# Kernel tuning notes

Measured on AMD Instinct MI355X. Metric: run time of the kernel, lower is better.

The kernel has to match this reference:

```python
import jax, jax.numpy as jnp
import numpy as np

B, C, H, W, P = 16, 512, 64, 64, 32


def setup_inputs() -> dict:
    key = jax.random.key(0)
    k1, k2, k3 = jax.random.split(key, 3)
    inputs = jax.random.normal(k1, (B, C, H, W), dtype=jnp.float32)
    weight = jax.random.uniform(k2, (P, C, 1, 1), dtype=jnp.float32)
    smooth_factor = jax.random.normal(k3, (P,), dtype=jnp.float32)
    return {"inputs": inputs, "weight": weight, "smooth_factor": smooth_factor}


def reference(inputs, weight, smooth_factor):
    b, c, h, w = inputs.shape
    p = weight.shape[0]
    n = h * w
    centers = weight.reshape(p, c)                      # [P,C]
    x = inputs.reshape(b, c, n)                         # [B,C,N]

    # distance-based logits: 2<c,x> - |x|^2 - |c|^2, clamped at 0
    cx = jnp.einsum('pc,bcn->bpn', centers, x)          # [B,P,N]
    x_sq = jnp.sum(x * x, axis=1, keepdims=True)        # [B,1,N]
    c_sq = jnp.sum(centers * centers, axis=1)[None, :, None]  # [1,P,1]
    beta = jax.nn.sigmoid(smooth_factor)                # [P]
    logits = jnp.minimum(2.0 * cx - x_sq - c_sq, 0.0) / beta[None, :, None]
    assign = jax.nn.softmax(logits, axis=1)             # [B,P,N]

    # assignment-weighted pooling
    qx = jnp.einsum('bpn,bcn->bpc', assign, x)          # [B,P,C]
    sum_ass = jnp.clip(jnp.sum(assign, axis=2, keepdims=True), 1e-5)  # [B,P,1]
    sigma = jnp.sqrt(beta / 2.0)                        # [P]
    out = (qx / sum_ass - centers[None, :, :]) / sigma[None, :, None]

    # L2-normalize over channel dim (torch F.normalize, eps=1e-12)
    norm = jnp.sqrt(jnp.sum(out * out, axis=2, keepdims=True))
    outputs = out / jnp.maximum(norm, 1e-12)
    outputs_t = jnp.transpose(outputs, (0, 2, 1))       # [B,C,P]
    assign_map = assign.reshape(b, p, h, w)             # [B,P,H,W]
    return outputs_t, assign_map
```

## Files before the change

kernel.cpp:

```cpp
#include <hip/hip_runtime.h>

constexpr int BB = 16;
constexpr int CC = 512;
constexpr int PP = 32;
constexpr int NN = 4096;
constexpr int TN = 128;

using f32x4 = __attribute__((ext_vector_type(4))) float;
using bf16x8 = __attribute__((ext_vector_type(8))) short;

__device__ __forceinline__ ushort f2bf(float f) {
  unsigned u = __builtin_bit_cast(unsigned, f);
  u += 0x7FFFu + ((u >> 16) & 1u);
  return (ushort)(u >> 16);
}

__global__ __launch_bounds__(64) void prep_kernel(
    const float* __restrict__ w, const float* __restrict__ sf,
    float* __restrict__ beta, float* __restrict__ rbeta,
    float* __restrict__ csq, float* __restrict__ sum_ass) {
  int p = blockIdx.x;
  int t = threadIdx.x;
  if (t < 16) sum_ass[p * 16 + t] = 0.f;
  float s = 0.f;
  for (int i = t; i < CC; i += 64) {
    float v = w[p * CC + i];
    s = fmaf(v, v, s);
  }
#pragma unroll
  for (int off = 32; off; off >>= 1) s += __shfl_down(s, off);
  if (t == 0) {
    csq[p] = s;
    float e = __expf(-sf[p]);
    rbeta[p] = 1.f + e;
    beta[p] = 1.f / (1.f + e);
  }
}

__global__ __launch_bounds__(256) void assign_kernel(
    const float* __restrict__ x, const float* __restrict__ w,
    const float* __restrict__ rbeta, const float* __restrict__ csq,
    float* __restrict__ assign_out, float* __restrict__ sum_ass) {
  __shared__ float xs[64][132];
  __shared__ float cs[64][36];
  __shared__ float xsq_p[8][TN];

  int tid = threadIdx.x;
  int b = blockIdx.x >> 5;
  int n0 = (blockIdx.x & 31) * TN;

  int sc = tid >> 5;
  int sn = (tid & 31) << 2;
  int sp = tid >> 3;
  int sk = (tid & 7) << 2;

  int nq = (tid & 31) << 2;
  int pq = (tid >> 5) << 2;

  const float* xb = x + (size_t)b * CC * NN + n0;

  float acc[16];
#pragma unroll
  for (int i = 0; i < 16; ++i) acc[i] = 0.f;
  float xq0 = 0.f, xq1 = 0.f, xq2 = 0.f, xq3 = 0.f;

  float4 xr[8], w0v, w1v;
#pragma unroll
  for (int ps = 0; ps < 8; ++ps)
    xr[ps] = *(const float4*)&xb[(size_t)(sc + ps * 8) * NN + sn];
  w0v = *(const float4*)&w[(size_t)sp * CC + sk];
  w1v = *(const float4*)&w[(size_t)sp * CC + sk + 32];
#pragma unroll
  for (int ps = 0; ps < 8; ++ps) {
    *(float4*)&xs[sc + ps * 8][sn] = xr[ps];
    xq0 = fmaf(xr[ps].x, xr[ps].x, xq0);
    xq1 = fmaf(xr[ps].y, xr[ps].y, xq1);
    xq2 = fmaf(xr[ps].z, xr[ps].z, xq2);
    xq3 = fmaf(xr[ps].w, xr[ps].w, xq3);
  }
  cs[sk + 0][sp] = w0v.x; cs[sk + 1][sp] = w0v.y;
  cs[sk + 2][sp] = w0v.z; cs[sk + 3][sp] = w0v.w;
  cs[sk + 32][sp] = w1v.x; cs[sk + 33][sp] = w1v.y;
  cs[sk + 34][sp] = w1v.z; cs[sk + 35][sp] = w1v.w;
  __syncthreads();

  for (int c0 = 0; c0 < CC; c0 += 64) {
    bool more = (c0 + 64 < CC);
    if (more) {
#pragma unroll
      for (int ps = 0; ps < 8; ++ps)
        xr[ps] = *(const float4*)&xb[(size_t)(c0 + 64 + sc + ps * 8) * NN + sn];
      w0v = *(const float4*)&w[(size_t)sp * CC + c0 + 64 + sk];
      w1v = *(const float4*)&w[(size_t)sp * CC + c0 + 64 + sk + 32];
    }
#pragma unroll 8
    for (int k = 0; k < 64; ++k) {
      float4 xv = *(const float4*)&xs[k][nq];
      float4 av = *(const float4*)&cs[k][pq];
      acc[0]  = fmaf(av.x, xv.x, acc[0]);
      acc[1]  = fmaf(av.x, xv.y, acc[1]);
      acc[2]  = fmaf(av.x, xv.z, acc[2]);
      acc[3]  = fmaf(av.x, xv.w, acc[3]);
      acc[4]  = fmaf(av.y, xv.x, acc[4]);
      acc[5]  = fmaf(av.y, xv.y, acc[5]);
      acc[6]  = fmaf(av.y, xv.z, acc[6]);
      acc[7]  = fmaf(av.y, xv.w, acc[7]);
      acc[8]  = fmaf(av.z, xv.x, acc[8]);
      acc[9]  = fmaf(av.z, xv.y, acc[9]);
      acc[10] = fmaf(av.z, xv.z, acc[10]);
      acc[11] = fmaf(av.z, xv.w, acc[11]);
      acc[12] = fmaf(av.w, xv.x, acc[12]);
      acc[13] = fmaf(av.w, xv.y, acc[13]);
      acc[14] = fmaf(av.w, xv.z, acc[14]);
      acc[15] = fmaf(av.w, xv.w, acc[15]);
    }
    if (more) {
      __syncthreads();
#pragma unroll
      for (int ps = 0; ps < 8; ++ps) {
        *(float4*)&xs[sc + ps * 8][sn] = xr[ps];
        xq0 = fmaf(xr[ps].x, xr[ps].x, xq0);
        xq1 = fmaf(xr[ps].y, xr[ps].y, xq1);
        xq2 = fmaf(xr[ps].z, xr[ps].z, xq2);
        xq3 = fmaf(xr[ps].w, xr[ps].w, xq3);
      }
      cs[sk + 0][sp] = w0v.x; cs[sk + 1][sp] = w0v.y;
      cs[sk + 2][sp] = w0v.z; cs[sk + 3][sp] = w0v.w;
      cs[sk + 32][sp] = w1v.x; cs[sk + 33][sp] = w1v.y;
      cs[sk + 34][sp] = w1v.z; cs[sk + 35][sp] = w1v.w;
      __syncthreads();
    }
  }

  *(float4*)&xsq_p[sc][sn] = make_float4(xq0, xq1, xq2, xq3);
  __syncthreads();

  float xs0 = 0.f, xs1 = 0.f, xs2 = 0.f, xs3 = 0.f;
#pragma unroll
  for (int g = 0; g < 8; ++g) {
    float4 v = *(const float4*)&xsq_p[g][nq];
    xs0 += v.x; xs1 += v.y; xs2 += v.z; xs3 += v.w;
  }

  float* lgs = &xs[0][0];
#pragma unroll
  for (int j = 0; j < 4; ++j) {
    float csj = csq[pq + j], rbj = rbeta[pq + j];
    lgs[(nq + 0) * 37 + pq + j] = fminf(2.f * acc[j * 4 + 0] - xs0 - csj, 0.f) * rbj;
    lgs[(nq + 1) * 37 + pq + j] = fminf(2.f * acc[j * 4 + 1] - xs1 - csj, 0.f) * rbj;
    lgs[(nq + 2) * 37 + pq + j] = fminf(2.f * acc[j * 4 + 2] - xs2 - csj, 0.f) * rbj;
    lgs[(nq + 3) * 37 + pq + j] = fminf(2.f * acc[j * 4 + 3] - xs3 - csj, 0.f) * rbj;
  }
  __syncthreads();

  if (tid < TN) {
    float v[PP];
    float m = -3.4e38f;
#pragma unroll
    for (int p = 0; p < PP; ++p) {
      v[p] = lgs[tid * 37 + p];
      m = fmaxf(m, v[p]);
    }
    float s = 0.f;
#pragma unroll
    for (int p = 0; p < PP; ++p) {
      v[p] = __expf(v[p] - m);
      s += v[p];
    }
    float inv = 1.f / s;
#pragma unroll
    for (int p = 0; p < PP; ++p) lgs[tid * 37 + p] = v[p] * inv;
  }
  __syncthreads();

#pragma unroll
  for (int rep = 0; rep < 4; ++rep) {
    int idx = tid + rep * 256;
    int p = idx >> 5;
    int nf = (idx & 31) << 2;
    float a0 = lgs[(nf + 0) * 37 + p];
    float a1 = lgs[(nf + 1) * 37 + p];
    float a2 = lgs[(nf + 2) * 37 + p];
    float a3 = lgs[(nf + 3) * 37 + p];
    *(float4*)&assign_out[((size_t)b * PP + p) * NN + n0 + nf] =
        make_float4(a0, a1, a2, a3);
    float s = (a0 + a1) + (a2 + a3);
#pragma unroll
    for (int off = 16; off; off >>= 1) s += __shfl_down(s, off, 32);
    if ((tid & 31) == 0) atomicAdd(&sum_ass[b * PP + p], s);
  }
}

__global__ __launch_bounds__(256) void qx_kernel(
    const float* __restrict__ x, const float* __restrict__ assign,
    float* __restrict__ qx_part) {
  __shared__ ushort xbf[128][136];
  __shared__ ushort abf[32][136];

  int tid = threadIdx.x;
  int b = blockIdx.y;
  int kc = blockIdx.x >> 2;
  int ct = blockIdx.x & 3;
  int wv = tid >> 6, lane = tid & 63;
  int l15 = lane & 15, lg = lane >> 4;

  const float* xb = x + ((size_t)b * CC + ct * 128) * NN + kc * 512;
  const float* ab = assign + (size_t)b * PP * NN + kc * 512;

  int c_s = tid >> 1;
  int nh  = (tid & 1) << 6;
  int p_s = tid >> 3;
  int na  = (tid & 7) << 4;

  f32x4 acc[2][2];
#pragma unroll
  for (int i = 0; i < 2; ++i)
#pragma unroll
    for (int j = 0; j < 2; ++j) acc[i][j] = {0.f, 0.f, 0.f, 0.f};

  for (int ch = 0; ch < 4; ++ch) {
    int nb = ch * 128;
    if (ch) __syncthreads();
#pragma unroll
    for (int h = 0; h < 2; ++h) {
      float4 v[8];
#pragma unroll
      for (int i = 0; i < 8; ++i)
        v[i] = *(const float4*)&xb[(size_t)c_s * NN + nb + nh + h * 32 + i * 4];
#pragma unroll
      for (int i = 0; i < 8; ++i) {
        ushort4 u;
        u.x = f2bf(v[i].x); u.y = f2bf(v[i].y);
        u.z = f2bf(v[i].z); u.w = f2bf(v[i].w);
        *(ushort4*)&xbf[c_s][nh + h * 32 + i * 4] = u;
      }
    }
    {
      float4 v[4];
#pragma unroll
      for (int i = 0; i < 4; ++i)
        v[i] = *(const float4*)&ab[(size_t)p_s * NN + nb + na + i * 4];
#pragma unroll
      for (int i = 0; i < 4; ++i) {
        ushort4 u;
        u.x = f2bf(v[i].x); u.y = f2bf(v[i].y);
        u.z = f2bf(v[i].z); u.w = f2bf(v[i].w);
        *(ushort4*)&abf[p_s][na + i * 4] = u;
      }
    }
    __syncthreads();
#pragma unroll
    for (int ks = 0; ks < 4; ++ks) {
      int nf = ks * 32 + lg * 8;
      bf16x8 a0 = *(const bf16x8*)&abf[l15][nf];
      bf16x8 a1 = *(const bf16x8*)&abf[16 + l15][nf];
      bf16x8 b0 = *(const bf16x8*)&xbf[wv * 32 + l15][nf];
      bf16x8 b1 = *(const bf16x8*)&xbf[wv * 32 + 16 + l15][nf];
      acc[0][0] = __builtin_amdgcn_mfma_f32_16x16x32_bf16(a0, b0, acc[0][0], 0, 0, 0);
      acc[0][1] = __builtin_amdgcn_mfma_f32_16x16x32_bf16(a0, b1, acc[0][1], 0, 0, 0);
      acc[1][0] = __builtin_amdgcn_mfma_f32_16x16x32_bf16(a1, b0, acc[1][0], 0, 0, 0);
      acc[1][1] = __builtin_amdgcn_mfma_f32_16x16x32_bf16(a1, b1, acc[1][1], 0, 0, 0);
    }
  }

#pragma unroll
  for (int pf = 0; pf < 2; ++pf)
#pragma unroll
    for (int cf = 0; cf < 2; ++cf)
#pragma unroll
      for (int i = 0; i < 4; ++i) {
        int p = pf * 16 + lg * 4 + i;
        int c = ct * 128 + wv * 32 + cf * 16 + l15;
        qx_part[(((size_t)kc * BB + b) * PP + p) * CC + c] = acc[pf][cf][i];
      }
}

__global__ __launch_bounds__(256) void finalize_kernel(
    const float* __restrict__ qx_part, const float* __restrict__ w,
    const float* __restrict__ beta, const float* __restrict__ sum_ass,
    float* __restrict__ out_t) {
  int b = blockIdx.x >> 5;
  int p = blockIdx.x & 31;
  int tid = threadIdx.x;
  int wave = tid >> 6, lane = tid & 63;

  float inv_sa = 1.f / fmaxf(sum_ass[b * PP + p], 1e-5f);
  float rsig = rsqrtf(0.5f * beta[p]);

  int c0 = tid, c1 = tid + 256;
  float q0 = 0.f, q1 = 0.f;
#pragma unroll
  for (int kc = 0; kc < 8; ++kc) {
    const float* row = qx_part + (((size_t)kc * BB + b) * PP + p) * CC;
    q0 += row[c0];
    q1 += row[c1];
  }
  const float* wrow = w + (size_t)p * CC;
  float t0 = (q0 * inv_sa - wrow[c0]) * rsig;
  float t1 = (q1 * inv_sa - wrow[c1]) * rsig;

  float nr = t0 * t0 + t1 * t1;
#pragma unroll
  for (int off = 32; off; off >>= 1) nr += __shfl_down(nr, off);
  __shared__ float red[4];
  if (lane == 0) red[wave] = nr;
  __syncthreads();
  float norm2 = red[0] + red[1] + red[2] + red[3];
  float scale = 1.f / fmaxf(sqrtf(norm2), 1e-12f);

  float* ob = out_t + (size_t)b * CC * PP + p;
  ob[(size_t)c0 * PP] = t0 * scale;
  ob[(size_t)c1 * PP] = t1 * scale;
}

extern "C" void kernel_launch(void* const* d_in, const int* in_sizes, int n_in,
                              void* d_out, int out_size, void* d_ws,
                              size_t ws_size, hipStream_t stream) {
  const float* x = (const float*)d_in[0];
  const float* w = (const float*)d_in[1];
  const float* sf = (const float*)d_in[2];

  float* out_t = (float*)d_out;
  float* assign = out_t + (size_t)BB * CC * PP;

  float* ws = (float*)d_ws;
  float* beta = ws;
  float* rbeta = ws + 32;
  float* csq = ws + 64;
  float* sum_ass = ws + 96;
  float* qx_part = ws + 608;

  prep_kernel<<<PP, 64, 0, stream>>>(w, sf, beta, rbeta, csq, sum_ass);
  assign_kernel<<<BB * 32, 256, 0, stream>>>(x, w, rbeta, csq, assign,
                                             sum_ass);
  qx_kernel<<<dim3(32, BB), 256, 0, stream>>>(x, assign, qx_part);
  finalize_kernel<<<BB * PP, 256, 0, stream>>>(qx_part, w, beta, sum_ass,
                                               out_t);
}
```

Before: 87.67 us.

## Use split-bf16 MFMA for assign GEMM and register-resident softmax

Replaces the FP32 FMA outer-product GEMM in assign_kernel with bf16 MFMA instructions. Each float is split into hi and lo bf16 parts and three products are accumulated to keep near-fp32 accuracy. The operands are stored packed in LDS, and the softmax runs directly on the MFMA accumulators with cross-lane shuffles, so the LDS logits round-trip is gone. This trades extra packing ALU work, scattered transposed LDS writes and many shuffles for the squared-norm reduction against higher matrix throughput; launch bounds now request 3 blocks per CU.

```diff
diff --git a/kernel.cpp b/kernel.cpp
--- a/kernel.cpp
+++ b/kernel.cpp
@@ -8,11 +8,35 @@
 
 using f32x4 = __attribute__((ext_vector_type(4))) float;
 using bf16x8 = __attribute__((ext_vector_type(8))) short;
+typedef unsigned int uint;
 
 __device__ __forceinline__ ushort f2bf(float f) {
   unsigned u = __builtin_bit_cast(unsigned, f);
   u += 0x7FFFu + ((u >> 16) & 1u);
   return (ushort)(u >> 16);
+}
+
+__device__ __forceinline__ uint packbf(float f) {
+  uint u = __builtin_bit_cast(uint, f);
+  uint hi = (u + (0x7FFFu + ((u >> 16) & 1u))) >> 16;
+  float hif = __builtin_bit_cast(float, hi << 16);
+  float lof = f - hif;
+  uint ul = __builtin_bit_cast(uint, lof);
+  uint lo = (ul + (0x7FFFu + ((ul >> 16) & 1u))) >> 16;
+  return (lo << 16) | hi;
+}
+
+struct BfPair { bf16x8 hi, lo; };
+
+__device__ __forceinline__ BfPair unpack8(const uint* __restrict__ row, int co) {
+  uint4 a = *(const uint4*)(row + co);
+  uint4 b = *(const uint4*)(row + co + 4);
+  union { bf16x8 v; uint d[4]; } H, L;
+  H.d[0] = (a.x & 0xffffu) | (a.y << 16); L.d[0] = (a.x >> 16) | (a.y & 0xffff0000u);
+  H.d[1] = (a.z & 0xffffu) | (a.w << 16); L.d[1] = (a.z >> 16) | (a.w & 0xffff0000u);
+  H.d[2] = (b.x & 0xffffu) | (b.y << 16); L.d[2] = (b.x >> 16) | (b.y & 0xffff0000u);
+  H.d[3] = (b.z & 0xffffu) | (b.w << 16); L.d[3] = (b.z >> 16) | (b.w & 0xffff0000u);
+  return {H.v, L.v};
 }
 
 __global__ __launch_bounds__(64) void prep_kernel(
@@ -37,158 +61,196 @@
   }
 }
 
-__global__ __launch_bounds__(256) void assign_kernel(
+__global__ __launch_bounds__(256, 3) void assign_kernel(
     const float* __restrict__ x, const float* __restrict__ w,
     const float* __restrict__ rbeta, const float* __restrict__ csq,
     float* __restrict__ assign_out, float* __restrict__ sum_ass) {
-  __shared__ float xs[64][132];
-  __shared__ float cs[64][36];
-  __shared__ float xsq_p[8][TN];
+  __shared__ uint xpk[128][68];
+  __shared__ uint cpk[32][68];
+  __shared__ float xsqw[4][4][32];
+  __shared__ float xsqf[128];
 
   int tid = threadIdx.x;
+  int wv = tid >> 6, lane = tid & 63;
+  int l15 = lane & 15, lg = lane >> 4;
   int b = blockIdx.x >> 5;
   int n0 = (blockIdx.x & 31) * TN;
 
-  int sc = tid >> 5;
-  int sn = (tid & 31) << 2;
-  int sp = tid >> 3;
-  int sk = (tid & 7) << 2;
-
-  int nq = (tid & 31) << 2;
-  int pq = (tid >> 5) << 2;
-
-  const float* xb = x + (size_t)b * CC * NN + n0;
-
-  float acc[16];
-#pragma unroll
-  for (int i = 0; i < 16; ++i) acc[i] = 0.f;
-  float xq0 = 0.f, xq1 = 0.f, xq2 = 0.f, xq3 = 0.f;
-
-  float4 xr[8], w0v, w1v;
-#pragma unroll
-  for (int ps = 0; ps < 8; ++ps)
-    xr[ps] = *(const float4*)&xb[(size_t)(sc + ps * 8) * NN + sn];
-  w0v = *(const float4*)&w[(size_t)sp * CC + sk];
-  w1v = *(const float4*)&w[(size_t)sp * CC + sk + 32];
-#pragma unroll
-  for (int ps = 0; ps < 8; ++ps) {
-    *(float4*)&xs[sc + ps * 8][sn] = xr[ps];
-    xq0 = fmaf(xr[ps].x, xr[ps].x, xq0);
-    xq1 = fmaf(xr[ps].y, xr[ps].y, xq1);
-    xq2 = fmaf(xr[ps].z, xr[ps].z, xq2);
-    xq3 = fmaf(xr[ps].w, xr[ps].w, xq3);
-  }
-  cs[sk + 0][sp] = w0v.x; cs[sk + 1][sp] = w0v.y;
-  cs[sk + 2][sp] = w0v.z; cs[sk + 3][sp] = w0v.w;
-  cs[sk + 32][sp] = w1v.x; cs[sk + 33][sp] = w1v.y;
-  cs[sk + 34][sp] = w1v.z; cs[sk + 35][sp] = w1v.w;
+  int c_s = tid >> 2;
+  int q = tid & 3;
+  int p_s = tid >> 3;
+  int cq8 = (tid & 7) << 3;
+
+  const float* xb = x + (size_t)b * CC * NN + n0 + q * 32;
+  const float* wb = w + (size_t)p_s * CC + cq8;
+
+  f32x4 acc[2][2];
+#pragma unroll
+  for (int i = 0; i < 2; ++i)
+#pragma unroll
+    for (int j = 0; j < 2; ++j) acc[i][j] = {0.f, 0.f, 0.f, 0.f};
+  float sq[32];
+#pragma unroll
+  for (int i = 0; i < 32; ++i) sq[i] = 0.f;
+
+  float4 xr[8], wr0, wr1;
+#pragma unroll
+  for (int i = 0; i < 8; ++i)
+    xr[i] = *(const float4*)&xb[(size_t)c_s * NN + i * 4];
+  wr0 = *(const float4*)&wb[0];
+  wr1 = *(const float4*)&wb[4];
+#pragma unroll
+  for (int i = 0; i < 8; ++i) {
+    float4 v = xr[i];
+    sq[4 * i + 0] = fmaf(v.x, v.x, sq[4 * i + 0]);
+    sq[4 * i + 1] = fmaf(v.y, v.y, sq[4 * i + 1]);
+    sq[4 * i + 2] = fmaf(v.z, v.z, sq[4 * i + 2]);
+    sq[4 * i + 3] = fmaf(v.w, v.w, sq[4 * i + 3]);
+    int nr = q * 32 + i * 4;
+    xpk[nr + 0][c_s] = packbf(v.x);
+    xpk[nr + 1][c_s] = packbf(v.y);
+    xpk[nr + 2][c_s] = packbf(v.z);
+    xpk[nr + 3][c_s] = packbf(v.w);
+  }
+  {
+    uint4 u0 = {packbf(wr0.x), packbf(wr0.y), packbf(wr0.z), packbf(wr0.w)};
+    uint4 u1 = {packbf(wr1.x), packbf(wr1.y), packbf(wr1.z), packbf(wr1.w)};
+    *(uint4*)&cpk[p_s][cq8] = u0;
+    *(uint4*)&cpk[p_s][cq8 + 4] = u1;
+  }
   __syncthreads();
 
   for (int c0 = 0; c0 < CC; c0 += 64) {
     bool more = (c0 + 64 < CC);
     if (more) {
 #pragma unroll
-      for (int ps = 0; ps < 8; ++ps)
-        xr[ps] = *(const float4*)&xb[(size_t)(c0 + 64 + sc + ps * 8) * NN + sn];
-      w0v = *(const float4*)&w[(size_t)sp * CC + c0 + 64 + sk];
-      w1v = *(const float4*)&w[(size_t)sp * CC + c0 + 64 + sk + 32];
-    }
-#pragma unroll 8
-    for (int k = 0; k < 64; ++k) {
-      float4 xv = *(const float4*)&xs[k][nq];
-      float4 av = *(const float4*)&cs[k][pq];
-      acc[0]  = fmaf(av.x, xv.x, acc[0]);
-      acc[1]  = fmaf(av.x, xv.y, acc[1]);
-      acc[2]  = fmaf(av.x, xv.z, acc[2]);
-      acc[3]  = fmaf(av.x, xv.w, acc[3]);
-      acc[4]  = fmaf(av.y, xv.x, acc[4]);
-      acc[5]  = fmaf(av.y, xv.y, acc[5]);
-      acc[6]  = fmaf(av.y, xv.z, acc[6]);
-      acc[7]  = fmaf(av.y, xv.w, acc[7]);
-      acc[8]  = fmaf(av.z, xv.x, acc[8]);
-      acc[9]  = fmaf(av.z, xv.y, acc[9]);
-      acc[10] = fmaf(av.z, xv.z, acc[10]);
-      acc[11] = fmaf(av.z, xv.w, acc[11]);
-      acc[12] = fmaf(av.w, xv.x, acc[12]);
-      acc[13] = fmaf(av.w, xv.y, acc[13]);
-      acc[14] = fmaf(av.w, xv.z, acc[14]);
-      acc[15] = fmaf(av.w, xv.w, acc[15]);
+      for (int i = 0; i < 8; ++i)
+        xr[i] = *(const float4*)&xb[(size_t)(c0 + 64 + c_s) * NN + i * 4];
+      wr0 = *(const float4*)&wb[c0 + 64];
+      wr1 = *(const float4*)&wb[c0 + 64 + 4];
+    }
+#pragma unroll
+    for (int ks = 0; ks < 2; ++ks) {
+      int co = ks * 32 + lg * 8;
+      BfPair A0 = unpack8(&cpk[l15][0], co);
+      BfPair A1 = unpack8(&cpk[l15 + 16][0], co);
+      BfPair B0 = unpack8(&xpk[wv * 32 + l15][0], co);
+      BfPair B1 = unpack8(&xpk[wv * 32 + 16 + l15][0], co);
+      acc[0][0] = __builtin_amdgcn_mfma_f32_16x16x32_bf16(A0.hi, B0.hi, acc[0][0], 0, 0, 0);
+      acc[0][1] = __builtin_amdgcn_mfma_f32_16x16x32_bf16(A0.hi, B1.hi, acc[0][1], 0, 0, 0);
+      acc[1][0] = __builtin_amdgcn_mfma_f32_16x16x32_bf16(A1.hi, B0.hi, acc[1][0], 0, 0, 0);
+      acc[1][1] = __builtin_amdgcn_mfma_f32_16x16x32_bf16(A1.hi, B1.hi, acc[1][1], 0, 0, 0);
+      acc[0][0] = __builtin_amdgcn_mfma_f32_16x16x32_bf16(A0.hi, B0.lo, acc[0][0], 0, 0, 0);
+      acc[0][1] = __builtin_amdgcn_mfma_f32_16x16x32_bf16(A0.hi, B1.lo, acc[0][1], 0, 0, 0);
+      acc[1][0] = __builtin_amdgcn_mfma_f32_16x16x32_bf16(A1.hi, B0.lo, acc[1][0], 0, 0, 0);
+      acc[1][1] = __builtin_amdgcn_mfma_f32_16x16x32_bf16(A1.hi, B1.lo, acc[1][1], 0, 0, 0);
+      acc[0][0] = __builtin_amdgcn_mfma_f32_16x16x32_bf16(A0.lo, B0.hi, acc[0][0], 0, 0, 0);
+      acc[0][1] = __builtin_amdgcn_mfma_f32_16x16x32_bf16(A0.lo, B1.hi, acc[0][1], 0, 0, 0);
+      acc[1][0] = __builtin_amdgcn_mfma_f32_16x16x32_bf16(A1.lo, B0.hi, acc[1][0], 0, 0, 0);
+      acc[1][1] = __builtin_amdgcn_mfma_f32_16x16x32_bf16(A1.lo, B1.hi, acc[1][1], 0, 0, 0);
     }
     if (more) {
       __syncthreads();
 #pragma unroll
-      for (int ps = 0; ps < 8; ++ps) {
-        *(float4*)&xs[sc + ps * 8][sn] = xr[ps];
-        xq0 = fmaf(xr[ps].x, xr[ps].x, xq0);
-        xq1 = fmaf(xr[ps].y, xr[ps].y, xq1);
-        xq2 = fmaf(xr[ps].z, xr[ps].z, xq2);
-        xq3 = fmaf(xr[ps].w, xr[ps].w, xq3);
+      for (int i = 0; i < 8; ++i) {
+        float4 v = xr[i];
+        sq[4 * i + 0] = fmaf(v.x, v.x, sq[4 * i + 0]);
+        sq[4 * i + 1] = fmaf(v.y, v.y, sq[4 * i + 1]);
+        sq[4 * i + 2] = fmaf(v.z, v.z, sq[4 * i + 2]);
+        sq[4 * i + 3] = fmaf(v.w, v.w, sq[4 * i + 3]);
+        int nr = q * 32 + i * 4;
+        xpk[nr + 0][c_s] = packbf(v.x);
+        xpk[nr + 1][c_s] = packbf(v.y);
+        xpk[nr + 2][c_s] = packbf(v.z);
+        xpk[nr + 3][c_s] = packbf(v.w);
       }
-      cs[sk + 0][sp] = w0v.x; cs[sk + 1][sp] = w0v.y;
-      cs[sk + 2][sp] = w0v.z; cs[sk + 3][sp] = w0v.w;
-      cs[sk + 32][sp] = w1v.x; cs[sk + 33][sp] = w1v.y;
-      cs[sk + 34][sp] = w1v.z; cs[sk + 35][sp] = w1v.w;
+      uint4 u0 = {packbf(wr0.x), packbf(wr0.y), packbf(wr0.z), packbf(wr0.w)};
+      uint4 u1 = {packbf(wr1.x), packbf(wr1.y), packbf(wr1.z), packbf(wr1.w)};
+      *(uint4*)&cpk[p_s][cq8] = u0;
+      *(uint4*)&cpk[p_s][cq8 + 4] = u1;
       __syncthreads();
     }
   }
 
-  *(float4*)&xsq_p[sc][sn] = make_float4(xq0, xq1, xq2, xq3);
+#pragma unroll
+  for (int i = 0; i < 32; ++i) {
+    sq[i] += __shfl_xor(sq[i], 4);
+    sq[i] += __shfl_xor(sq[i], 8);
+    sq[i] += __shfl_xor(sq[i], 16);
+    sq[i] += __shfl_xor(sq[i], 32);
+  }
+  if ((lane >> 2) == 0) {
+#pragma unroll
+    for (int i = 0; i < 32; ++i) xsqw[wv][lane & 3][i] = sq[i];
+  }
   __syncthreads();
-
-  float xs0 = 0.f, xs1 = 0.f, xs2 = 0.f, xs3 = 0.f;
-#pragma unroll
-  for (int g = 0; g < 8; ++g) {
-    float4 v = *(const float4*)&xsq_p[g][nq];
-    xs0 += v.x; xs1 += v.y; xs2 += v.z; xs3 += v.w;
-  }
-
-  float* lgs = &xs[0][0];
-#pragma unroll
-  for (int j = 0; j < 4; ++j) {
-    float csj = csq[pq + j], rbj = rbeta[pq + j];
-    lgs[(nq + 0) * 37 + pq + j] = fminf(2.f * acc[j * 4 + 0] - xs0 - csj, 0.f) * rbj;
-    lgs[(nq + 1) * 37 + pq + j] = fminf(2.f * acc[j * 4 + 1] - xs1 - csj, 0.f) * rbj;
-    lgs[(nq + 2) * 37 + pq + j] = fminf(2.f * acc[j * 4 + 2] - xs2 - csj, 0.f) * rbj;
-    lgs[(nq + 3) * 37 + pq + j] = fminf(2.f * acc[j * 4 + 3] - xs3 - csj, 0.f) * rbj;
-  }
+  if (tid < 128)
+    xsqf[tid] = xsqw[0][tid >> 5][tid & 31] + xsqw[1][tid >> 5][tid & 31] +
+                xsqw[2][tid >> 5][tid & 31] + xsqw[3][tid >> 5][tid & 31];
   __syncthreads();
 
-  if (tid < TN) {
-    float v[PP];
-    float m = -3.4e38f;
-#pragma unroll
-    for (int p = 0; p < PP; ++p) {
-      v[p] = lgs[tid * 37 + p];
-      m = fmaxf(m, v[p]);
-    }
-    float s = 0.f;
-#pragma unroll
-    for (int p = 0; p < PP; ++p) {
-      v[p] = __expf(v[p] - m);
-      s += v[p];
-    }
-    float inv = 1.f / s;
-#pragma unroll
-    for (int p = 0; p < PP; ++p) lgs[tid * 37 + p] = v[p] * inv;
-  }
-  __syncthreads();
-
-#pragma unroll
-  for (int rep = 0; rep < 4; ++rep) {
-    int idx = tid + rep * 256;
-    int p = idx >> 5;
-    int nf = (idx & 31) << 2;
-    float a0 = lgs[(nf + 0) * 37 + p];
-    float a1 = lgs[(nf + 1) * 37 + p];
-    float a2 = lgs[(nf + 2) * 37 + p];
-    float a3 = lgs[(nf + 3) * 37 + p];
-    *(float4*)&assign_out[((size_t)b * PP + p) * NN + n0 + nf] =
-        make_float4(a0, a1, a2, a3);
-    float s = (a0 + a1) + (a2 + a3);
-#pragma unroll
-    for (int off = 16; off; off >>= 1) s += __shfl_down(s, off, 32);
-    if ((tid & 31) == 0) atomicAdd(&sum_ass[b * PP + p], s);
-  }
+  float xsqn0 = xsqf[wv * 32 + l15];
+  float xsqn1 = xsqf[wv * 32 + 16 + l15];
+
+  float csqv[2][4], rbv[2][4];
+#pragma unroll
+  for (int pf = 0; pf < 2; ++pf)
+#pragma unroll
+    for (int i = 0; i < 4; ++i) {
+      int p = pf * 16 + lg * 4 + i;
+      csqv[pf][i] = csq[p];
+      rbv[pf][i] = rbeta[p];
+    }
+
+  float L[2][2][4];
+  float m0 = -3.4e38f, m1 = -3.4e38f;
+#pragma unroll
+  for (int pf = 0; pf < 2; ++pf)
+#pragma unroll
+    for (int i = 0; i < 4; ++i) {
+      float l0 = fminf(2.f * acc[pf][0][i] - xsqn0 - csqv[pf][i], 0.f) * rbv[pf][i];
+      float l1 = fminf(2.f * acc[pf][1][i] - xsqn1 - csqv[pf][i], 0.f) * rbv[pf][i];
+      L[pf][0][i] = l0; L[pf][1][i] = l1;
+      m0 = fmaxf(m0, l0); m1 = fmaxf(m1, l1);
+    }
+  m0 = fmaxf(m0, __shfl_xor(m0, 16)); m0 = fmaxf(m0, __shfl_xor(m0, 32));
+  m1 = fmaxf(m1, __shfl_xor(m1, 16)); m1 = fmaxf(m1, __shfl_xor(m1, 32));
+  float s0 = 0.f, s1 = 0.f;
+#pragma unroll
+  for (int pf = 0; pf < 2; ++pf)
+#pragma unroll
+    for (int i = 0; i < 4; ++i) {
+      float e0 = __expf(L[pf][0][i] - m0);
+      float e1 = __expf(L[pf][1][i] - m1);
+      L[pf][0][i] = e0; L[pf][1][i] = e1;
+      s0 += e0; s1 += e1;
+    }
+  s0 += __shfl_xor(s0, 16); s0 += __shfl_xor(s0, 32);
+  s1 += __shfl_xor(s1, 16); s1 += __shfl_xor(s1, 32);
+  float inv0 = 1.f / s0, inv1 = 1.f / s1;
+
+  float* aoB = assign_out + (size_t)b * PP * NN + n0 + wv * 32 + l15;
+  float sa[2][4];
+#pragma unroll
+  for (int pf = 0; pf < 2; ++pf)
+#pragma unroll
+    for (int i = 0; i < 4; ++i) {
+      int p = pf * 16 + lg * 4 + i;
+      float a0 = L[pf][0][i] * inv0;
+      float a1 = L[pf][1][i] * inv1;
+      aoB[(size_t)p * NN] = a0;
+      aoB[(size_t)p * NN + 16] = a1;
+      sa[pf][i] = a0 + a1;
+    }
+#pragma unroll
+  for (int pf = 0; pf < 2; ++pf)
+#pragma unroll
+    for (int i = 0; i < 4; ++i) {
+      float v = sa[pf][i];
+      v += __shfl_xor(v, 1); v += __shfl_xor(v, 2);
+      v += __shfl_xor(v, 4); v += __shfl_xor(v, 8);
+      if (l15 == 0) atomicAdd(&sum_ass[b * PP + pf * 16 + lg * 4 + i], v);
+    }
 }
 
 __global__ __launch_bounds__(256) void qx_kernel(
```

Measured after the change: 88.89 us. Within noise of the previous version (+1.4%).

## Compute assignment logits with split-bf16 MFMA and in-register softmax

Applied to the files above, without the earlier changes.

The assign kernel's FP32 FMA GEMM through shared memory is replaced by bf16 MFMA 16x16x32 instructions. A hi/lo split of both centers and x, using three products, keeps precision close to fp32. The prep kernel now precomputes the hi/lo bf16 center splits into workspace. Softmax over P is done with cross-lane shuffles in registers, with no LDS staging or block barriers. The risks are that x is read straight from global memory with strided scalar loads and no LDS reuse, and that the split drops the lo*lo term.

```diff
diff --git a/kernel.cpp b/kernel.cpp
--- a/kernel.cpp
+++ b/kernel.cpp
@@ -4,10 +4,10 @@
 constexpr int CC = 512;
 constexpr int PP = 32;
 constexpr int NN = 4096;
-constexpr int TN = 128;
 
 using f32x4 = __attribute__((ext_vector_type(4))) float;
 using bf16x8 = __attribute__((ext_vector_type(8))) short;
+typedef unsigned int uint;
 
 __device__ __forceinline__ ushort f2bf(float f) {
   unsigned u = __builtin_bit_cast(unsigned, f);
@@ -18,15 +18,28 @@
 __global__ __launch_bounds__(64) void prep_kernel(
     const float* __restrict__ w, const float* __restrict__ sf,
     float* __restrict__ beta, float* __restrict__ rbeta,
-    float* __restrict__ csq, float* __restrict__ sum_ass) {
+    float* __restrict__ csq, float* __restrict__ sum_ass,
+    ushort* __restrict__ chi, ushort* __restrict__ clo) {
   int p = blockIdx.x;
   int t = threadIdx.x;
   if (t < 16) sum_ass[p * 16 + t] = 0.f;
   float s = 0.f;
-  for (int i = t; i < CC; i += 64) {
-    float v = w[p * CC + i];
-    s = fmaf(v, v, s);
-  }
+  int c8 = t * 8;
+  float4 v0 = *(const float4*)&w[p * CC + c8];
+  float4 v1 = *(const float4*)&w[p * CC + c8 + 4];
+  ushort h[8], l[8];
+  float vv[8] = {v0.x, v0.y, v0.z, v0.w, v1.x, v1.y, v1.z, v1.w};
+#pragma unroll
+  for (int i = 0; i < 8; ++i) {
+    s = fmaf(vv[i], vv[i], s);
+    h[i] = f2bf(vv[i]);
+    float hf = __builtin_bit_cast(float, (uint)h[i] << 16);
+    l[i] = f2bf(vv[i] - hf);
+  }
+  *(ushort4*)&chi[p * CC + c8] = make_ushort4(h[0], h[1], h[2], h[3]);
+  *(ushort4*)&chi[p * CC + c8 + 4] = make_ushort4(h[4], h[5], h[6], h[7]);
+  *(ushort4*)&clo[p * CC + c8] = make_ushort4(l[0], l[1], l[2], l[3]);
+  *(ushort4*)&clo[p * CC + c8 + 4] = make_ushort4(l[4], l[5], l[6], l[7]);
 #pragma unroll
   for (int off = 32; off; off >>= 1) s += __shfl_down(s, off);
   if (t == 0) {
@@ -38,157 +51,122 @@
 }
 
 __global__ __launch_bounds__(256) void assign_kernel(
-    const float* __restrict__ x, const float* __restrict__ w,
-    const float* __restrict__ rbeta, const float* __restrict__ csq,
-    float* __restrict__ assign_out, float* __restrict__ sum_ass) {
-  __shared__ float xs[64][132];
-  __shared__ float cs[64][36];
-  __shared__ float xsq_p[8][TN];
-
+    const float* __restrict__ x, const ushort* __restrict__ chi,
+    const ushort* __restrict__ clo, const float* __restrict__ rbeta_,
+    const float* __restrict__ csq_, float* __restrict__ assign_out,
+    float* __restrict__ sum_ass) {
   int tid = threadIdx.x;
+  int wv = tid >> 6, lane = tid & 63;
+  int l15 = lane & 15, lg = lane >> 4;
   int b = blockIdx.x >> 5;
-  int n0 = (blockIdx.x & 31) * TN;
-
-  int sc = tid >> 5;
-  int sn = (tid & 31) << 2;
-  int sp = tid >> 3;
-  int sk = (tid & 7) << 2;
-
-  int nq = (tid & 31) << 2;
-  int pq = (tid >> 5) << 2;
-
-  const float* xb = x + (size_t)b * CC * NN + n0;
-
-  float acc[16];
-#pragma unroll
-  for (int i = 0; i < 16; ++i) acc[i] = 0.f;
-  float xq0 = 0.f, xq1 = 0.f, xq2 = 0.f, xq3 = 0.f;
-
-  float4 xr[8], w0v, w1v;
-#pragma unroll
-  for (int ps = 0; ps < 8; ++ps)
-    xr[ps] = *(const float4*)&xb[(size_t)(sc + ps * 8) * NN + sn];
-  w0v = *(const float4*)&w[(size_t)sp * CC + sk];
-  w1v = *(const float4*)&w[(size_t)sp * CC + sk + 32];
-#pragma unroll
-  for (int ps = 0; ps < 8; ++ps) {
-    *(float4*)&xs[sc + ps * 8][sn] = xr[ps];
-    xq0 = fmaf(xr[ps].x, xr[ps].x, xq0);
-    xq1 = fmaf(xr[ps].y, xr[ps].y, xq1);
-    xq2 = fmaf(xr[ps].z, xr[ps].z, xq2);
-    xq3 = fmaf(xr[ps].w, xr[ps].w, xq3);
-  }
-  cs[sk + 0][sp] = w0v.x; cs[sk + 1][sp] = w0v.y;
-  cs[sk + 2][sp] = w0v.z; cs[sk + 3][sp] = w0v.w;
-  cs[sk + 32][sp] = w1v.x; cs[sk + 33][sp] = w1v.y;
-  cs[sk + 34][sp] = w1v.z; cs[sk + 35][sp] = w1v.w;
-  __syncthreads();
-
-  for (int c0 = 0; c0 < CC; c0 += 64) {
-    bool more = (c0 + 64 < CC);
-    if (more) {
-#pragma unroll
-      for (int ps = 0; ps < 8; ++ps)
-        xr[ps] = *(const float4*)&xb[(size_t)(c0 + 64 + sc + ps * 8) * NN + sn];
-      w0v = *(const float4*)&w[(size_t)sp * CC + c0 + 64 + sk];
-      w1v = *(const float4*)&w[(size_t)sp * CC + c0 + 64 + sk + 32];
-    }
-#pragma unroll 8
-    for (int k = 0; k < 64; ++k) {
-      float4 xv = *(const float4*)&xs[k][nq];
-      float4 av = *(const float4*)&cs[k][pq];
-      acc[0]  = fmaf(av.x, xv.x, acc[0]);
-      acc[1]  = fmaf(av.x, xv.y, acc[1]);
-      acc[2]  = fmaf(av.x, xv.z, acc[2]);
-      acc[3]  = fmaf(av.x, xv.w, acc[3]);
-      acc[4]  = fmaf(av.y, xv.x, acc[4]);
-      acc[5]  = fmaf(av.y, xv.y, acc[5]);
-      acc[6]  = fmaf(av.y, xv.z, acc[6]);
-      acc[7]  = fmaf(av.y, xv.w, acc[7]);
-      acc[8]  = fmaf(av.z, xv.x, acc[8]);
-      acc[9]  = fmaf(av.z, xv.y, acc[9]);
-      acc[10] = fmaf(av.z, xv.z, acc[10]);
-      acc[11] = fmaf(av.z, xv.w, acc[11]);
-      acc[12] = fmaf(av.w, xv.x, acc[12]);
-      acc[13] = fmaf(av.w, xv.y, acc[13]);
-      acc[14] = fmaf(av.w, xv.z, acc[14]);
-      acc[15] = fmaf(av.w, xv.w, acc[15]);
-    }
-    if (more) {
-      __syncthreads();
-#pragma unroll
-      for (int ps = 0; ps < 8; ++ps) {
-        *(float4*)&xs[sc + ps * 8][sn] = xr[ps];
-        xq0 = fmaf(xr[ps].x, xr[ps].x, xq0);
-        xq1 = fmaf(xr[ps].y, xr[ps].y, xq1);
-        xq2 = fmaf(xr[ps].z, xr[ps].z, xq2);
-        xq3 = fmaf(xr[ps].w, xr[ps].w, xq3);
-      }
-      cs[sk + 0][sp] = w0v.x; cs[sk + 1][sp] = w0v.y;
-      cs[sk + 2][sp] = w0v.z; cs[sk + 3][sp] = w0v.w;
-      cs[sk + 32][sp] = w1v.x; cs[sk + 33][sp] = w1v.y;
-      cs[sk + 34][sp] = w1v.z; cs[sk + 35][sp] = w1v.w;
-      __syncthreads();
-    }
-  }
-
-  *(float4*)&xsq_p[sc][sn] = make_float4(xq0, xq1, xq2, xq3);
-  __syncthreads();
-
-  float xs0 = 0.f, xs1 = 0.f, xs2 = 0.f, xs3 = 0.f;
-#pragma unroll
-  for (int g = 0; g < 8; ++g) {
-    float4 v = *(const float4*)&xsq_p[g][nq];
-    xs0 += v.x; xs1 += v.y; xs2 += v.z; xs3 += v.w;
-  }
-
-  float* lgs = &xs[0][0];
-#pragma unroll
-  for (int j = 0; j < 4; ++j) {
-    float csj = csq[pq + j], rbj = rbeta[pq + j];
-    lgs[(nq + 0) * 37 + pq + j] = fminf(2.f * acc[j * 4 + 0] - xs0 - csj, 0.f) * rbj;
-    lgs[(nq + 1) * 37 + pq + j] = fminf(2.f * acc[j * 4 + 1] - xs1 - csj, 0.f) * rbj;
-    lgs[(nq + 2) * 37 + pq + j] = fminf(2.f * acc[j * 4 + 2] - xs2 - csj, 0.f) * rbj;
-    lgs[(nq + 3) * 37 + pq + j] = fminf(2.f * acc[j * 4 + 3] - xs3 - csj, 0.f) * rbj;
-  }
-  __syncthreads();
-
-  if (tid < TN) {
-    float v[PP];
-    float m = -3.4e38f;
-#pragma unroll
-    for (int p = 0; p < PP; ++p) {
-      v[p] = lgs[tid * 37 + p];
-      m = fmaxf(m, v[p]);
-    }
-    float s = 0.f;
-#pragma unroll
-    for (int p = 0; p < PP; ++p) {
-      v[p] = __expf(v[p] - m);
-      s += v[p];
-    }
-    float inv = 1.f / s;
-#pragma unroll
-    for (int p = 0; p < PP; ++p) lgs[tid * 37 + p] = v[p] * inv;
-  }
-  __syncthreads();
-
-#pragma unroll
-  for (int rep = 0; rep < 4; ++rep) {
-    int idx = tid + rep * 256;
-    int p = idx >> 5;
-    int nf = (idx & 31) << 2;
-    float a0 = lgs[(nf + 0) * 37 + p];
-    float a1 = lgs[(nf + 1) * 37 + p];
-    float a2 = lgs[(nf + 2) * 37 + p];
-    float a3 = lgs[(nf + 3) * 37 + p];
-    *(float4*)&assign_out[((size_t)b * PP + p) * NN + n0 + nf] =
-        make_float4(a0, a1, a2, a3);
-    float s = (a0 + a1) + (a2 + a3);
-#pragma unroll
-    for (int off = 16; off; off >>= 1) s += __shfl_down(s, off, 32);
-    if ((tid & 31) == 0) atomicAdd(&sum_ass[b * PP + p], s);
-  }
+  int n0 = (blockIdx.x & 31) * 128 + wv * 32;
+
+  const float* xb = x + (size_t)b * CC * NN + n0 + l15;
+
+  f32x4 acc[2][2];
+#pragma unroll
+  for (int i = 0; i < 2; ++i)
+#pragma unroll
+    for (int j = 0; j < 2; ++j) acc[i][j] = {0.f, 0.f, 0.f, 0.f};
+  float xsq[2] = {0.f, 0.f};
+
+#pragma unroll 4
+  for (int ks = 0; ks < 16; ++ks) {
+    int c0 = ks * 32 + lg * 8;
+    bf16x8 Ah0 = *(const bf16x8*)&chi[l15 * CC + c0];
+    bf16x8 Ah1 = *(const bf16x8*)&chi[(l15 + 16) * CC + c0];
+    bf16x8 Al0 = *(const bf16x8*)&clo[l15 * CC + c0];
+    bf16x8 Al1 = *(const bf16x8*)&clo[(l15 + 16) * CC + c0];
+#pragma unroll
+    for (int nf = 0; nf < 2; ++nf) {
+      float xv[8];
+#pragma unroll
+      for (int j = 0; j < 8; ++j)
+        xv[j] = xb[(size_t)(c0 + j) * NN + nf * 16];
+      union { bf16x8 v; ushort e[8]; } Bh, Bl;
+#pragma unroll
+      for (int j = 0; j < 8; ++j) {
+        xsq[nf] = fmaf(xv[j], xv[j], xsq[nf]);
+        ushort h = f2bf(xv[j]);
+        float hf = __builtin_bit_cast(float, (uint)h << 16);
+        Bh.e[j] = h;
+        Bl.e[j] = f2bf(xv[j] - hf);
+      }
+      acc[0][nf] = __builtin_amdgcn_mfma_f32_16x16x32_bf16(Ah0, Bh.v, acc[0][nf], 0, 0, 0);
+      acc[1][nf] = __builtin_amdgcn_mfma_f32_16x16x32_bf16(Ah1, Bh.v, acc[1][nf], 0, 0, 0);
+      acc[0][nf] = __builtin_amdgcn_mfma_f32_16x16x32_bf16(Ah0, Bl.v, acc[0][nf], 0, 0, 0);
+      acc[1][nf] = __builtin_amdgcn_mfma_f32_16x16x32_bf16(Ah1, Bl.v, acc[1][nf], 0, 0, 0);
+      acc[0][nf] = __builtin_amdgcn_mfma_f32_16x16x32_bf16(Al0, Bh.v, acc[0][nf], 0, 0, 0);
+      acc[1][nf] = __builtin_amdgcn_mfma_f32_16x16x32_bf16(Al1, Bh.v, acc[1][nf], 0, 0, 0);
+    }
+  }
+
+#pragma unroll
+  for (int nf = 0; nf < 2; ++nf) {
+    xsq[nf] += __shfl_xor(xsq[nf], 16);
+    xsq[nf] += __shfl_xor(xsq[nf], 32);
+  }
+
+  float csqv[2][4], rbv[2][4];
+#pragma unroll
+  for (int pf = 0; pf < 2; ++pf)
+#pragma unroll
+    for (int i = 0; i < 4; ++i) {
+      int p = pf * 16 + lg * 4 + i;
+      csqv[pf][i] = csq_[p];
+      rbv[pf][i] = rbeta_[p];
+    }
+
+  float L[2][2][4];
+  float m[2] = {-3.4e38f, -3.4e38f};
+#pragma unroll
+  for (int pf = 0; pf < 2; ++pf)
+#pragma unroll
+    for (int nf = 0; nf < 2; ++nf)
+#pragma unroll
+      for (int i = 0; i < 4; ++i) {
+        float l = fminf(2.f * acc[pf][nf][i] - xsq[nf] - csqv[pf][i], 0.f) * rbv[pf][i];
+        L[pf][nf][i] = l;
+        m[nf] = fmaxf(m[nf], l);
+      }
+#pragma unroll
+  for (int nf = 0; nf < 2; ++nf) {
+    m[nf] = fmaxf(m[nf], __shfl_xor(m[nf], 16));
+    m[nf] = fmaxf(m[nf], __shfl_xor(m[nf], 32));
+  }
+  float s[2] = {0.f, 0.f};
+#pragma unroll
+  for (int pf = 0; pf < 2; ++pf)
+#pragma unroll
+    for (int nf = 0; nf < 2; ++nf)
+#pragma unroll
+      for (int i = 0; i < 4; ++i) {
+        float e = __expf(L[pf][nf][i] - m[nf]);
+        L[pf][nf][i] = e;
+        s[nf] += e;
+      }
+#pragma unroll
+  for (int nf = 0; nf < 2; ++nf) {
+    s[nf] += __shfl_xor(s[nf], 16);
+    s[nf] += __shfl_xor(s[nf], 32);
+    s[nf] = 1.f / s[nf];
+  }
+
+  float* aoB = assign_out + (size_t)b * PP * NN + n0 + l15;
+#pragma unroll
+  for (int pf = 0; pf < 2; ++pf)
+#pragma unroll
+    for (int i = 0; i < 4; ++i) {
+      int p = pf * 16 + lg * 4 + i;
+      float a0 = L[pf][0][i] * s[0];
+      float a1 = L[pf][1][i] * s[1];
+      aoB[(size_t)p * NN] = a0;
+      aoB[(size_t)p * NN + 16] = a1;
+      float v = a0 + a1;
+      v += __shfl_xor(v, 1); v += __shfl_xor(v, 2);
+      v += __shfl_xor(v, 4); v += __shfl_xor(v, 8);
+      if (l15 == 0) atomicAdd(&sum_ass[b * PP + p], v);
+    }
 }
 
 __global__ __launch_bounds__(256) void qx_kernel(
@@ -329,10 +307,13 @@
   float* csq = ws + 64;
   float* sum_ass = ws + 96;
   float* qx_part = ws + 608;
-
-  prep_kernel<<<PP, 64, 0, stream>>>(w, sf, beta, rbeta, csq, sum_ass);
-  assign_kernel<<<BB * 32, 256, 0, stream>>>(x, w, rbeta, csq, assign,
-                                             sum_ass);
+  ushort* chi = (ushort*)(ws + 608 + 2097152);
+  ushort* clo = chi + PP * CC;
+
+  prep_kernel<<<PP, 64, 0, stream>>>(w, sf, beta, rbeta, csq, sum_ass,
+                                     chi, clo);
+  assign_kernel<<<512, 256, 0, stream>>>(x, chi, clo, rbeta, csq, assign,
+                                         sum_ass);
   qx_kernel<<<dim3(32, BB), 256, 0, stream>>>(x, assign, qx_part);
   finalize_kernel<<<BB * PP, 256, 0, stream>>>(qx_part, w, beta, sum_ass,
                                                out_t);
```

Result: faster. 85.66 us, median of 2 (-2.3%).
